# Kernel optimization log

Measured on AMD Instinct MI355X. Metric: run time of the kernel, lower is better.

The kernel has to match this reference:

```python
import jax, jax.numpy as jnp
import numpy as np

B, T, C = 2, 2048, 1024
R = 16
LORA_SCALE = 1.0 / R  # lora_alpha(=1) / r


def lora_linear(x, w, b, a, bb):
    # loralib: y = x @ W^T + bias + (x @ A^T) @ B^T * scaling
    return x @ w.T + b + (x @ a.T) @ bb.T * LORA_SCALE


def setup_inputs() -> dict:
    key = jax.random.key(0)
    ks = jax.random.split(key, 8)
    s = 0.02
    return {
        "x": jax.random.normal(ks[0], (B, T, C), jnp.float32),
        "w_attn": jax.random.normal(ks[1], (3 * C, C), jnp.float32) * s,
        "b_attn": jnp.zeros((3 * C,), jnp.float32),
        "lora_a_attn": jax.random.normal(ks[2], (R, C), jnp.float32) * s,
        "lora_b_attn": jnp.zeros((3 * C, R), jnp.float32),
        "w_proj": jax.random.normal(ks[3], (C, C), jnp.float32) * s,
        "b_proj": jnp.zeros((C,), jnp.float32),
        "lora_a_proj": jax.random.normal(ks[4], (R, C), jnp.float32) * s,
        "lora_b_proj": jnp.zeros((C, R), jnp.float32),
        "n_head": 16,
    }


def reference(x, w_attn, b_attn, lora_a_attn, lora_b_attn, w_proj, b_proj,
              lora_a_proj, lora_b_proj, n_head):
    b, t, c = x.shape
    hd = c // n_head
    qkv = lora_linear(x, w_attn, b_attn, lora_a_attn, lora_b_attn)
    q, k, v = jnp.split(qkv, 3, axis=2)
    # (B, H, T, hd)
    q = q.reshape(b, t, n_head, hd).transpose(0, 2, 1, 3)
    k = k.reshape(b, t, n_head, hd).transpose(0, 2, 1, 3)
    v = v.reshape(b, t, n_head, hd).transpose(0, 2, 1, 3)
    att = jnp.einsum("bhqd,bhkd->bhqk", q, k) * (1.0 / np.sqrt(hd).astype(np.float32))
    causal = jnp.tril(jnp.ones((t, t), bool))
    att = jnp.where(causal[None, None], att, jnp.float32(-jnp.inf))
    att = jax.nn.softmax(att, axis=-1)
    y = jnp.einsum("bhqk,bhkd->bhqd", att, v)
    y = y.transpose(0, 2, 1, 3).reshape(b, t, c)
    return lora_linear(y, w_proj, b_proj, lora_a_proj, lora_b_proj)
```

## Files before the change

### kernel.cpp

```cpp
#include <hip/hip_runtime.h>

typedef __attribute__((ext_vector_type(8))) short bf16x8;
typedef __attribute__((ext_vector_type(4))) short bf16x4;
typedef __attribute__((ext_vector_type(4))) float f32x4;

__device__ __forceinline__ float bf2f(unsigned short u) {
    unsigned int x = ((unsigned int)u) << 16;
    float f;
    __builtin_memcpy(&f, &x, 4);
    return f;
}
__device__ __forceinline__ unsigned short f2bf(float f) {
    unsigned int x;
    __builtin_memcpy(&x, &f, 4);
    x += 0x7FFFu + ((x >> 16) & 1u);
    return (unsigned short)(x >> 16);
}

#define GLOAD_LDS16(gp, lp)                                      \
    __builtin_amdgcn_global_load_lds(                            \
        (const __attribute__((address_space(1))) void*)(gp),     \
        (__attribute__((address_space(3))) void*)(lp), 16, 0, 0)

__global__ __launch_bounds__(256) void prep(
    const float* __restrict__ x, unsigned short* __restrict__ xb,
    const float* __restrict__ w_attn, const float* __restrict__ la_attn,
    const float* __restrict__ lb_attn, unsigned short* __restrict__ Weff_attn,
    const float* __restrict__ w_proj, const float* __restrict__ la_proj,
    const float* __restrict__ lb_proj, unsigned short* __restrict__ Weff_proj) {
    const int bid = blockIdx.x;
    if (bid < 2048) {
        int i = (bid * 256 + threadIdx.x) * 8;
        float4 v0 = *(const float4*)(x + i);
        float4 v1 = *(const float4*)(x + i + 4);
        bf16x8 o;
        o[0] = (short)f2bf(v0.x); o[1] = (short)f2bf(v0.y);
        o[2] = (short)f2bf(v0.z); o[3] = (short)f2bf(v0.w);
        o[4] = (short)f2bf(v1.x); o[5] = (short)f2bf(v1.y);
        o[6] = (short)f2bf(v1.z); o[7] = (short)f2bf(v1.w);
        *(bf16x8*)(xb + i) = o;
        return;
    }
    const float* W;
    const float* Ain;
    const float* Bin;
    unsigned short* Weff;
    int idx;
    if (bid < 3584) {
        idx = ((bid - 2048) * 256 + threadIdx.x) * 8;
        W = w_attn; Ain = la_attn; Bin = lb_attn; Weff = Weff_attn;
    } else {
        idx = ((bid - 3584) * 256 + threadIdx.x) * 8;
        W = w_proj; Ain = la_proj; Bin = lb_proj; Weff = Weff_proj;
    }
    const int n = idx >> 10;
    const int k = idx & 1023;
    float s[8];
#pragma unroll
    for (int j = 0; j < 8; ++j) s[j] = 0.f;
#pragma unroll
    for (int r = 0; r < 16; ++r) {
        const float bcoef = Bin[n * 16 + r];
        float4 a0 = *(const float4*)(Ain + r * 1024 + k);
        float4 a1 = *(const float4*)(Ain + r * 1024 + k + 4);
        s[0] += bcoef * a0.x; s[1] += bcoef * a0.y;
        s[2] += bcoef * a0.z; s[3] += bcoef * a0.w;
        s[4] += bcoef * a1.x; s[5] += bcoef * a1.y;
        s[6] += bcoef * a1.z; s[7] += bcoef * a1.w;
    }
    float4 w0 = *(const float4*)(W + idx);
    float4 w1 = *(const float4*)(W + idx + 4);
    bf16x8 o;
    o[0] = (short)f2bf(w0.x + 0.0625f * s[0]);
    o[1] = (short)f2bf(w0.y + 0.0625f * s[1]);
    o[2] = (short)f2bf(w0.z + 0.0625f * s[2]);
    o[3] = (short)f2bf(w0.w + 0.0625f * s[3]);
    o[4] = (short)f2bf(w1.x + 0.0625f * s[4]);
    o[5] = (short)f2bf(w1.y + 0.0625f * s[5]);
    o[6] = (short)f2bf(w1.z + 0.0625f * s[6]);
    o[7] = (short)f2bf(w1.w + 0.0625f * s[7]);
    *(bf16x8*)(Weff + idx) = o;
}

template <bool F32OUT, bool VSPLIT>
__global__ __launch_bounds__(256) void gemm_bt_bias(
    const unsigned short* __restrict__ A, const unsigned short* __restrict__ B,
    const float* __restrict__ bias, unsigned short* __restrict__ Cb,
    float* __restrict__ Cf, unsigned short* __restrict__ Vtout,
    int M, int N, int K) {
    __shared__ unsigned short sA0[128 * 32], sA1[128 * 32];
    __shared__ unsigned short sB0[128 * 32], sB1[128 * 32];
    const int tid = threadIdx.x;
    const int wave = tid >> 6, lane = tid & 63;
    const int quad = lane >> 4, l16 = lane & 15;
    const int m0 = blockIdx.y * 128, n0 = blockIdx.x * 128;
    const int wm = (wave & 1) * 64, wn = (wave >> 1) * 64;

    const int srow = wave * 32 + (lane >> 2);
    const int scol = (lane & 3) * 8;
    const unsigned short* Ag = A + (size_t)(m0 + srow) * K + scol;
    const unsigned short* Bg = B + (size_t)(n0 + srow) * K + scol;
    const int woff = wave * 1024;
    const size_t kjump = (size_t)16 * K;

    f32x4 acc[4][4];
#pragma unroll
    for (int i = 0; i < 4; ++i)
#pragma unroll
        for (int j = 0; j < 4; ++j) acc[i][j] = (f32x4){0.f, 0.f, 0.f, 0.f};

    auto stage = [&](unsigned short* dA, unsigned short* dB, int k) {
        GLOAD_LDS16(Ag + k, dA + woff);
        GLOAD_LDS16(Ag + k + kjump, dA + woff + 512);
        GLOAD_LDS16(Bg + k, dB + woff);
        GLOAD_LDS16(Bg + k + kjump, dB + woff + 512);
    };
    auto compute = [&](const unsigned short* cA, const unsigned short* cB) {
        bf16x8 af[4], bfr[4];
#pragma unroll
        for (int mi = 0; mi < 4; ++mi)
            af[mi] = *(const bf16x8*)&cA[(wm + mi * 16 + l16) * 32 + quad * 8];
#pragma unroll
        for (int ni = 0; ni < 4; ++ni)
            bfr[ni] = *(const bf16x8*)&cB[(wn + ni * 16 + l16) * 32 + quad * 8];
#pragma unroll
        for (int mi = 0; mi < 4; ++mi)
#pragma unroll
            for (int ni = 0; ni < 4; ++ni)
                acc[mi][ni] = __builtin_amdgcn_mfma_f32_16x16x32_bf16(
                    af[mi], bfr[ni], acc[mi][ni], 0, 0, 0);
    };

    stage(sA0, sB0, 0);
    __syncthreads();
    for (int k0 = 0; k0 < K; k0 += 64) {
        if (k0 + 32 < K) stage(sA1, sB1, k0 + 32);
        compute(sA0, sB0);
        __syncthreads();
        if (k0 + 64 < K) stage(sA0, sB0, k0 + 64);
        compute(sA1, sB1);
        __syncthreads();
    }

    float bv[4];
#pragma unroll
    for (int ni = 0; ni < 4; ++ni) bv[ni] = bias[n0 + wn + ni * 16 + l16];

    if (VSPLIT && n0 >= 2048) {
#pragma unroll
        for (int ni = 0; ni < 4; ++ni) {
            const int hcol = n0 + wn + ni * 16 + l16 - 2048;
#pragma unroll
            for (int mi = 0; mi < 4; ++mi) {
                const int rowtop = m0 + wm + mi * 16 + quad * 4;
                const int bb = rowtop >> 11;
                const int t = rowtop & 2047;
                bf16x4 pk;
#pragma unroll
                for (int r = 0; r < 4; ++r)
                    pk[r] = (short)f2bf(acc[mi][ni][r] + bv[ni]);
                *(bf16x4*)(Vtout +
                           ((size_t)((bb * 16 + (hcol >> 6)) * 64 + (hcol & 63))) *
                               2048 +
                           t) = pk;
            }
        }
        return;
    }

#pragma unroll
    for (int mi = 0; mi < 4; ++mi)
#pragma unroll
        for (int ni = 0; ni < 4; ++ni)
#pragma unroll
            for (int r = 0; r < 4; ++r) {
                int row = m0 + wm + mi * 16 + quad * 4 + r;
                int col = n0 + wn + ni * 16 + l16;
                float val = acc[mi][ni][r] + bv[ni];
                if (F32OUT)
                    Cf[(size_t)row * N + col] = val;
                else
                    Cb[(size_t)row * N + col] = f2bf(val);
            }
}

__global__ __launch_bounds__(256) void gemm_bt_bias64(
    const unsigned short* __restrict__ A, const unsigned short* __restrict__ B,
    const float* __restrict__ bias, float* __restrict__ Cf,
    int M, int N, int K) {
    __shared__ unsigned short sA0[64 * 32], sA1[64 * 32];
    __shared__ unsigned short sB0[128 * 32], sB1[128 * 32];
    const int tid = threadIdx.x;
    const int wave = tid >> 6, lane = tid & 63;
    const int quad = lane >> 4, l16 = lane & 15;
    const int m0 = blockIdx.y * 64, n0 = blockIdx.x * 128;
    const int wn = wave * 32;

    const int srowA = wave * 16 + (lane >> 2);
    const int srowB = wave * 32 + (lane >> 2);
    const int scol = (lane & 3) * 8;
    const unsigned short* Ag = A + (size_t)(m0 + srowA) * K + scol;
    const unsigned short* Bg = B + (size_t)(n0 + srowB) * K + scol;
    const int woffA = wave * 512, woffB = wave * 1024;
    const size_t kjump = (size_t)16 * K;

    f32x4 acc[4][2];
#pragma unroll
    for (int i = 0; i < 4; ++i)
#pragma unroll
        for (int j = 0; j < 2; ++j) acc[i][j] = (f32x4){0.f, 0.f, 0.f, 0.f};

    auto stage = [&](unsigned short* dA, unsigned short* dB, int k) {
        GLOAD_LDS16(Ag + k, dA + woffA);
        GLOAD_LDS16(Bg + k, dB + woffB);
        GLOAD_LDS16(Bg + k + kjump, dB + woffB + 512);
    };
    auto compute = [&](const unsigned short* cA, const unsigned short* cB) {
        bf16x8 af[4], bfr[2];
#pragma unroll
        for (int mi = 0; mi < 4; ++mi)
            af[mi] = *(const bf16x8*)&cA[(mi * 16 + l16) * 32 + quad * 8];
#pragma unroll
        for (int ni = 0; ni < 2; ++ni)
            bfr[ni] = *(const bf16x8*)&cB[(wn + ni * 16 + l16) * 32 + quad * 8];
#pragma unroll
        for (int mi = 0; mi < 4; ++mi)
#pragma unroll
            for (int ni = 0; ni < 2; ++ni)
                acc[mi][ni] = __builtin_amdgcn_mfma_f32_16x16x32_bf16(
                    af[mi], bfr[ni], acc[mi][ni], 0, 0, 0);
    };

    stage(sA0, sB0, 0);
    __syncthreads();
    for (int k0 = 0; k0 < K; k0 += 64) {
        if (k0 + 32 < K) stage(sA1, sB1, k0 + 32);
        compute(sA0, sB0);
        __syncthreads();
        if (k0 + 64 < K) stage(sA0, sB0, k0 + 64);
        compute(sA1, sB1);
        __syncthreads();
    }

    float bv[2];
#pragma unroll
    for (int ni = 0; ni < 2; ++ni) bv[ni] = bias[n0 + wn + ni * 16 + l16];
#pragma unroll
    for (int mi = 0; mi < 4; ++mi)
#pragma unroll
        for (int ni = 0; ni < 2; ++ni)
#pragma unroll
            for (int r = 0; r < 4; ++r) {
                int row = m0 + mi * 16 + quad * 4 + r;
                int col = n0 + wn + ni * 16 + l16;
                Cf[(size_t)row * N + col] = acc[mi][ni][r] + bv[ni];
            }
}

__global__ __launch_bounds__(256) void attn_kernel(
    const unsigned short* __restrict__ qkv,
    const unsigned short* __restrict__ Vt,
    unsigned short* __restrict__ y) {
    const int b = blockIdx.z, h = blockIdx.y;
    const int bh = b * 16 + h;
    const int qblk = (int)blockIdx.x ^ (((bh >> 3) & 1) ? 31 : 0);
    const int w = threadIdx.x >> 6, lane = threadIdx.x & 63;
    const int quad = lane >> 4, l16 = lane & 15;
    const int q0 = qblk * 64 + w * 16;
    const int ntiles = qblk + 1;

    __shared__ unsigned short sK[64 * 72];
    __shared__ unsigned short sV[64 * 72];
    __shared__ unsigned short sP[4][16 * 72];

    const unsigned short* Qb = qkv + (size_t)(b * 2048) * 3072 + h * 64;
    const unsigned short* Kg = Qb + 1024;
    const unsigned short* Vg = Vt + (size_t)(bh * 64) * 2048;

    const int rlo = threadIdx.x >> 3;
    const int c8 = (threadIdx.x & 7) * 8;

    bf16x8 qf0 = *(const bf16x8*)(Qb + (size_t)(q0 + l16) * 3072 + quad * 8);
    bf16x8 qf1 = *(const bf16x8*)(Qb + (size_t)(q0 + l16) * 3072 + 32 + quad * 8);

    f32x4 o[4];
    float lacc = 0.f;
#pragma unroll
    for (int nt = 0; nt < 4; ++nt) o[nt] = (f32x4){0.f, 0.f, 0.f, 0.f};

    const float csc = 0.125f * 1.44269504088896340736f;

    bf16x8 kr0 = *(const bf16x8*)(Kg + (size_t)rlo * 3072 + c8);
    bf16x8 kr1 = *(const bf16x8*)(Kg + (size_t)(rlo + 32) * 3072 + c8);
    bf16x8 vr0 = *(const bf16x8*)(Vg + (size_t)rlo * 2048 + c8);
    bf16x8 vr1 = *(const bf16x8*)(Vg + (size_t)(rlo + 32) * 2048 + c8);

    for (int it = 0; it < ntiles; ++it) {
        const int kv0 = it * 64;
        __syncthreads();
        *(bf16x8*)&sK[rlo * 72 + c8] = kr0;
        *(bf16x8*)&sK[(rlo + 32) * 72 + c8] = kr1;
        *(bf16x8*)&sV[rlo * 72 + c8] = vr0;
        *(bf16x8*)&sV[(rlo + 32) * 72 + c8] = vr1;
        __syncthreads();
        if (it + 1 < ntiles) {
            const int nx = kv0 + 64;
            kr0 = *(const bf16x8*)(Kg + (size_t)(nx + rlo) * 3072 + c8);
            kr1 = *(const bf16x8*)(Kg + (size_t)(nx + rlo + 32) * 3072 + c8);
            vr0 = *(const bf16x8*)(Vg + (size_t)rlo * 2048 + nx + c8);
            vr1 = *(const bf16x8*)(Vg + (size_t)(rlo + 32) * 2048 + nx + c8);
        }

        f32x4 S[4];
#pragma unroll
        for (int f = 0; f < 4; ++f) {
            bf16x8 klo = *(const bf16x8*)&sK[(f * 16 + l16) * 72 + quad * 8];
            bf16x8 khi = *(const bf16x8*)&sK[(f * 16 + l16) * 72 + 32 + quad * 8];
            S[f] = (f32x4){0.f, 0.f, 0.f, 0.f};
            S[f] = __builtin_amdgcn_mfma_f32_16x16x32_bf16(klo, qf0, S[f], 0, 0, 0);
            S[f] = __builtin_amdgcn_mfma_f32_16x16x32_bf16(khi, qf1, S[f], 0, 0, 0);
        }
        const bool diag = (it == qblk);
        const int qr16 = w * 16 + l16;
#pragma unroll
        for (int f = 0; f < 4; ++f) {
            float p0, p1, p2, p3;
            {
                float sv = S[f][0] * csc;
                asm("v_exp_f32 %0, %1" : "=v"(p0) : "v"(sv));
                sv = S[f][1] * csc;
                asm("v_exp_f32 %0, %1" : "=v"(p1) : "v"(sv));
                sv = S[f][2] * csc;
                asm("v_exp_f32 %0, %1" : "=v"(p2) : "v"(sv));
                sv = S[f][3] * csc;
                asm("v_exp_f32 %0, %1" : "=v"(p3) : "v"(sv));
            }
            if (diag) {
                int c = f * 16 + quad * 4;
                p0 = (c + 0 <= qr16) ? p0 : 0.f;
                p1 = (c + 1 <= qr16) ? p1 : 0.f;
                p2 = (c + 2 <= qr16) ? p2 : 0.f;
                p3 = (c + 3 <= qr16) ? p3 : 0.f;
            }
            lacc += (p0 + p1) + (p2 + p3);
            unsigned int d0, d1;
            asm("v_cvt_pk_bf16_f32 %0, %1, %2" : "=v"(d0) : "v"(p0), "v"(p1));
            asm("v_cvt_pk_bf16_f32 %0, %1, %2" : "=v"(d1) : "v"(p2), "v"(p3));
            *(uint2*)&sP[w][l16 * 72 + f * 16 + quad * 4] = (uint2){d0, d1};
        }
        asm volatile("" ::: "memory");
        bf16x8 pf0 = *(const bf16x8*)&sP[w][l16 * 72 + quad * 8];
        bf16x8 pf1 = *(const bf16x8*)&sP[w][l16 * 72 + 32 + quad * 8];
#pragma unroll
        for (int nt = 0; nt < 4; ++nt) {
            bf16x8 v0 = *(const bf16x8*)&sV[(nt * 16 + l16) * 72 + quad * 8];
            bf16x8 v1 = *(const bf16x8*)&sV[(nt * 16 + l16) * 72 + 32 + quad * 8];
            o[nt] = __builtin_amdgcn_mfma_f32_16x16x32_bf16(pf0, v0, o[nt], 0, 0, 0);
            o[nt] = __builtin_amdgcn_mfma_f32_16x16x32_bf16(pf1, v1, o[nt], 0, 0, 0);
        }
    }

    lacc += __shfl_xor(lacc, 16);
    lacc += __shfl_xor(lacc, 32);
    float lt[4];
#pragma unroll
    for (int r = 0; r < 4; ++r) lt[r] = __shfl(lacc, quad * 4 + r);

    unsigned short* yb = y + (size_t)(b * 2048) * 1024 + h * 64;
#pragma unroll
    for (int nt = 0; nt < 4; ++nt)
#pragma unroll
        for (int r = 0; r < 4; ++r)
            yb[(size_t)(q0 + quad * 4 + r) * 1024 + nt * 16 + l16] =
                f2bf(o[nt][r] / lt[r]);
}

extern "C" void kernel_launch(void* const* d_in, const int* in_sizes, int n_in,
                              void* d_out, int out_size, void* d_ws, size_t ws_size,
                              hipStream_t stream) {
    const float* x       = (const float*)d_in[0];
    const float* w_attn  = (const float*)d_in[1];
    const float* b_attn  = (const float*)d_in[2];
    const float* la_attn = (const float*)d_in[3];
    const float* lb_attn = (const float*)d_in[4];
    const float* w_proj  = (const float*)d_in[5];
    const float* b_proj  = (const float*)d_in[6];
    const float* la_proj = (const float*)d_in[7];
    const float* lb_proj = (const float*)d_in[8];
    float* out = (float*)d_out;

    char* w = (char*)d_ws;
    unsigned short* xb        = (unsigned short*)w; w += (size_t)4096 * 1024 * 2;
    unsigned short* Weff_attn = (unsigned short*)w; w += (size_t)3072 * 1024 * 2;
    unsigned short* Weff_proj = (unsigned short*)w; w += (size_t)1024 * 1024 * 2;
    unsigned short* qkv       = (unsigned short*)w; w += (size_t)4096 * 3072 * 2;
    unsigned short* Vt        = (unsigned short*)w; w += (size_t)32 * 64 * 2048 * 2;
    unsigned short* y         = (unsigned short*)w; w += (size_t)4096 * 1024 * 2;

    prep<<<4096, 256, 0, stream>>>(x, xb, w_attn, la_attn, lb_attn, Weff_attn,
                                   w_proj, la_proj, lb_proj, Weff_proj);
    gemm_bt_bias<false, true><<<dim3(24, 32), 256, 0, stream>>>(
        xb, Weff_attn, b_attn, qkv, (float*)nullptr, Vt, 4096, 3072, 1024);
    attn_kernel<<<dim3(32, 16, 2), 256, 0, stream>>>(qkv, Vt, y);
    gemm_bt_bias64<<<dim3(8, 64), 256, 0, stream>>>(
        y, Weff_proj, b_proj, out, 4096, 1024, 1024);
}
```

Baseline: 188.1 us.

## Split attention warps across query and KV halves, keep P in registers

The attention kernel's warp partition changes. Each warp now handles 32 query rows and one half of each 64-key tile, instead of 16 query rows and the full tile. The S accumulator rows are permuted with a krow0 mapping so that the exp'd probabilities can be packed straight into the MFMA A-operand, which removes the per-tile LDS round trip through sP. The two KV-half partial outputs and denominators are merged through shared memory at the end. The cost is a final reduction step with two extra barriers, more accumulator registers, and a launch_bounds occupancy hint of 4.

```diff
diff --git a/kernel.cpp b/kernel.cpp
--- a/kernel.cpp
+++ b/kernel.cpp
@@ -257,7 +257,7 @@
             }
 }
 
-__global__ __launch_bounds__(256) void attn_kernel(
+__global__ __launch_bounds__(256, 4) void attn_kernel(
     const unsigned short* __restrict__ qkv,
     const unsigned short* __restrict__ Vt,
     unsigned short* __restrict__ y) {
@@ -266,12 +266,15 @@
     const int qblk = (int)blockIdx.x ^ (((bh >> 3) & 1) ? 31 : 0);
     const int w = threadIdx.x >> 6, lane = threadIdx.x & 63;
     const int quad = lane >> 4, l16 = lane & 15;
-    const int q0 = qblk * 64 + w * 16;
+    const int qh = w & 1, kvh = w >> 1;
+    const int q0 = qblk * 64 + qh * 32;
     const int ntiles = qblk + 1;
 
-    __shared__ unsigned short sK[64 * 72];
-    __shared__ unsigned short sV[64 * 72];
-    __shared__ unsigned short sP[4][16 * 72];
+    __shared__ __align__(16) char smem[18432 + 512];
+    unsigned short* sK = (unsigned short*)smem;
+    unsigned short* sV = sK + 64 * 72;
+    float* sO = (float*)smem;
+    float* sD = (float*)(smem + 18432);
 
     const unsigned short* Qb = qkv + (size_t)(b * 2048) * 3072 + h * 64;
     const unsigned short* Kg = Qb + 1024;
@@ -280,13 +283,21 @@
     const int rlo = threadIdx.x >> 3;
     const int c8 = (threadIdx.x & 7) * 8;
 
-    bf16x8 qf0 = *(const bf16x8*)(Qb + (size_t)(q0 + l16) * 3072 + quad * 8);
-    bf16x8 qf1 = *(const bf16x8*)(Qb + (size_t)(q0 + l16) * 3072 + 32 + quad * 8);
-
-    f32x4 o[4];
-    float lacc = 0.f;
-#pragma unroll
-    for (int nt = 0; nt < 4; ++nt) o[nt] = (f32x4){0.f, 0.f, 0.f, 0.f};
+    bf16x8 qf[2][2];
+#pragma unroll
+    for (int m = 0; m < 2; ++m) {
+        qf[m][0] = *(const bf16x8*)(Qb + (size_t)(q0 + m * 16 + l16) * 3072 + quad * 8);
+        qf[m][1] = *(const bf16x8*)(Qb + (size_t)(q0 + m * 16 + l16) * 3072 + 32 + quad * 8);
+    }
+
+    const int krow0 = kvh * 32 + 8 * (l16 >> 2) + (l16 & 3);
+
+    f32x4 o[2][4];
+    float lacc[2] = {0.f, 0.f};
+#pragma unroll
+    for (int m = 0; m < 2; ++m)
+#pragma unroll
+        for (int nt = 0; nt < 4; ++nt) o[m][nt] = (f32x4){0.f, 0.f, 0.f, 0.f};
 
     const float csc = 0.125f * 1.44269504088896340736f;
 
@@ -311,68 +322,102 @@
             vr1 = *(const bf16x8*)(Vg + (size_t)(rlo + 32) * 2048 + nx + c8);
         }
 
-        f32x4 S[4];
-#pragma unroll
-        for (int f = 0; f < 4; ++f) {
-            bf16x8 klo = *(const bf16x8*)&sK[(f * 16 + l16) * 72 + quad * 8];
-            bf16x8 khi = *(const bf16x8*)&sK[(f * 16 + l16) * 72 + 32 + quad * 8];
-            S[f] = (f32x4){0.f, 0.f, 0.f, 0.f};
-            S[f] = __builtin_amdgcn_mfma_f32_16x16x32_bf16(klo, qf0, S[f], 0, 0, 0);
-            S[f] = __builtin_amdgcn_mfma_f32_16x16x32_bf16(khi, qf1, S[f], 0, 0, 0);
+        bf16x8 ka[2][2];
+#pragma unroll
+        for (int f = 0; f < 2; ++f) {
+            ka[f][0] = *(const bf16x8*)&sK[(krow0 + 4 * f) * 72 + quad * 8];
+            ka[f][1] = *(const bf16x8*)&sK[(krow0 + 4 * f) * 72 + 32 + quad * 8];
         }
+        bf16x8 vb[4];
+#pragma unroll
+        for (int nt = 0; nt < 4; ++nt)
+            vb[nt] = *(const bf16x8*)&sV[(nt * 16 + l16) * 72 + kvh * 32 + quad * 8];
+
         const bool diag = (it == qblk);
-        const int qr16 = w * 16 + l16;
-#pragma unroll
-        for (int f = 0; f < 4; ++f) {
-            float p0, p1, p2, p3;
-            {
-                float sv = S[f][0] * csc;
-                asm("v_exp_f32 %0, %1" : "=v"(p0) : "v"(sv));
-                sv = S[f][1] * csc;
-                asm("v_exp_f32 %0, %1" : "=v"(p1) : "v"(sv));
-                sv = S[f][2] * csc;
-                asm("v_exp_f32 %0, %1" : "=v"(p2) : "v"(sv));
-                sv = S[f][3] * csc;
-                asm("v_exp_f32 %0, %1" : "=v"(p3) : "v"(sv));
+#pragma unroll
+        for (int m = 0; m < 2; ++m) {
+            const int qa = q0 + m * 16 + l16;
+            unsigned int pw[4];
+            float lsum = 0.f;
+#pragma unroll
+            for (int f = 0; f < 2; ++f) {
+                f32x4 S = (f32x4){0.f, 0.f, 0.f, 0.f};
+                S = __builtin_amdgcn_mfma_f32_16x16x32_bf16(ka[f][0], qf[m][0], S, 0, 0, 0);
+                S = __builtin_amdgcn_mfma_f32_16x16x32_bf16(ka[f][1], qf[m][1], S, 0, 0, 0);
+                float p0, p1, p2, p3;
+                {
+                    float sv = S[0] * csc;
+                    asm("v_exp_f32 %0, %1" : "=v"(p0) : "v"(sv));
+                    sv = S[1] * csc;
+                    asm("v_exp_f32 %0, %1" : "=v"(p1) : "v"(sv));
+                    sv = S[2] * csc;
+                    asm("v_exp_f32 %0, %1" : "=v"(p2) : "v"(sv));
+                    sv = S[3] * csc;
+                    asm("v_exp_f32 %0, %1" : "=v"(p3) : "v"(sv));
+                }
+                if (diag) {
+                    int kvb = kv0 + kvh * 32 + 8 * quad + 4 * f;
+                    p0 = (kvb + 0 <= qa) ? p0 : 0.f;
+                    p1 = (kvb + 1 <= qa) ? p1 : 0.f;
+                    p2 = (kvb + 2 <= qa) ? p2 : 0.f;
+                    p3 = (kvb + 3 <= qa) ? p3 : 0.f;
+                }
+                lsum += (p0 + p1) + (p2 + p3);
+                asm("v_cvt_pk_bf16_f32 %0, %1, %2" : "=v"(pw[f * 2 + 0]) : "v"(p0), "v"(p1));
+                asm("v_cvt_pk_bf16_f32 %0, %1, %2" : "=v"(pw[f * 2 + 1]) : "v"(p2), "v"(p3));
             }
-            if (diag) {
-                int c = f * 16 + quad * 4;
-                p0 = (c + 0 <= qr16) ? p0 : 0.f;
-                p1 = (c + 1 <= qr16) ? p1 : 0.f;
-                p2 = (c + 2 <= qr16) ? p2 : 0.f;
-                p3 = (c + 3 <= qr16) ? p3 : 0.f;
+            lacc[m] += lsum;
+            union {
+                unsigned int u[4];
+                bf16x8 v;
+            } pa;
+            pa.u[0] = pw[0]; pa.u[1] = pw[1]; pa.u[2] = pw[2]; pa.u[3] = pw[3];
+#pragma unroll
+            for (int nt = 0; nt < 4; ++nt)
+                o[m][nt] = __builtin_amdgcn_mfma_f32_16x16x32_bf16(
+                    pa.v, vb[nt], o[m][nt], 0, 0, 0);
+        }
+    }
+
+#pragma unroll
+    for (int m = 0; m < 2; ++m) {
+        lacc[m] += __shfl_xor(lacc[m], 16);
+        lacc[m] += __shfl_xor(lacc[m], 32);
+    }
+
+    __syncthreads();
+    if (kvh == 1) {
+        float* dst = sO + qh * (64 * 36);
+#pragma unroll
+        for (int m = 0; m < 2; ++m)
+#pragma unroll
+            for (int nt = 0; nt < 4; ++nt)
+                *(f32x4*)&dst[(nt * 16 + l16) * 36 + m * 16 + quad * 4] = o[m][nt];
+    }
+    if (lane < 16) {
+        sD[w * 32 + l16] = lacc[0];
+        sD[w * 32 + 16 + l16] = lacc[1];
+    }
+    __syncthreads();
+    if (kvh == 0) {
+        const float* src = sO + qh * (64 * 36);
+        unsigned short* yb = y + (size_t)(b * 2048) * 1024 + h * 64;
+#pragma unroll
+        for (int m = 0; m < 2; ++m) {
+            float dfull = lacc[m] + sD[(w + 2) * 32 + m * 16 + l16];
+            float lt[4];
+#pragma unroll
+            for (int r = 0; r < 4; ++r) lt[r] = __shfl(dfull, quad * 4 + r);
+#pragma unroll
+            for (int nt = 0; nt < 4; ++nt) {
+                f32x4 part = *(const f32x4*)&src[(nt * 16 + l16) * 36 + m * 16 + quad * 4];
+#pragma unroll
+                for (int r = 0; r < 4; ++r)
+                    yb[(size_t)(q0 + m * 16 + quad * 4 + r) * 1024 + nt * 16 + l16] =
+                        f2bf((o[m][nt][r] + part[r]) / lt[r]);
             }
-            lacc += (p0 + p1) + (p2 + p3);
-            unsigned int d0, d1;
-            asm("v_cvt_pk_bf16_f32 %0, %1, %2" : "=v"(d0) : "v"(p0), "v"(p1));
-            asm("v_cvt_pk_bf16_f32 %0, %1, %2" : "=v"(d1) : "v"(p2), "v"(p3));
-            *(uint2*)&sP[w][l16 * 72 + f * 16 + quad * 4] = (uint2){d0, d1};
         }
-        asm volatile("" ::: "memory");
-        bf16x8 pf0 = *(const bf16x8*)&sP[w][l16 * 72 + quad * 8];
-        bf16x8 pf1 = *(const bf16x8*)&sP[w][l16 * 72 + 32 + quad * 8];
-#pragma unroll
-        for (int nt = 0; nt < 4; ++nt) {
-            bf16x8 v0 = *(const bf16x8*)&sV[(nt * 16 + l16) * 72 + quad * 8];
-            bf16x8 v1 = *(const bf16x8*)&sV[(nt * 16 + l16) * 72 + 32 + quad * 8];
-            o[nt] = __builtin_amdgcn_mfma_f32_16x16x32_bf16(pf0, v0, o[nt], 0, 0, 0);
-            o[nt] = __builtin_amdgcn_mfma_f32_16x16x32_bf16(pf1, v1, o[nt], 0, 0, 0);
-        }
-    }
-
-    lacc += __shfl_xor(lacc, 16);
-    lacc += __shfl_xor(lacc, 32);
-    float lt[4];
-#pragma unroll
-    for (int r = 0; r < 4; ++r) lt[r] = __shfl(lacc, quad * 4 + r);
-
-    unsigned short* yb = y + (size_t)(b * 2048) * 1024 + h * 64;
-#pragma unroll
-    for (int nt = 0; nt < 4; ++nt)
-#pragma unroll
-        for (int r = 0; r < 4; ++r)
-            yb[(size_t)(q0 + quad * 4 + r) * 1024 + nt * 16 + l16] =
-                f2bf(o[nt][r] / lt[r]);
+    }
 }
 
 extern "C" void kernel_launch(void* const* d_in, const int* in_sizes, int n_in,
```

New measurement: 188.6 us. About the same (+0.3%).
